# Kernel optimization log

Measured on AMD Instinct MI355X. Metric: run time of the kernel, lower is better.

## Reference

```python
import jax, jax.numpy as jnp
import numpy as np

B, N, D = 8, 1024, 768      # batch, n_patches, prototype dim
V, C, Hh = 30000, 512, 768  # vocab size, clip_text_dim, proj hidden dim
TEMPERATURE = 0.2
BN_EPS = 1e-5


def _l2norm(x, axis=-1, eps=1e-12):
    # matches torch F.normalize (clamp_min on the norm)
    n = jnp.linalg.norm(x, axis=axis, keepdims=True)
    return x / jnp.maximum(n, eps)


def setup_inputs() -> dict:
    key = jax.random.key(0)
    k = jax.random.split(key, 6)
    patch_tokens = jax.random.normal(k[0], (B, N, D), dtype=jnp.float32)
    vocab_clip_embeddings = jax.random.normal(k[1], (V, C), dtype=jnp.float32)
    # ProjectionHead params: Linear(C->Hh, no bias) + BN(Hh) + ReLU + Linear(Hh->D, bias)
    W1 = jax.random.normal(k[2], (C, Hh), dtype=jnp.float32) / np.sqrt(C)
    bn_gamma = jnp.ones((Hh,), dtype=jnp.float32)
    bn_beta = jnp.zeros((Hh,), dtype=jnp.float32)
    W2 = jax.random.normal(k[3], (Hh, D), dtype=jnp.float32) / np.sqrt(Hh)
    b2 = jnp.zeros((D,), dtype=jnp.float32)
    return {
        "patch_tokens": patch_tokens,
        "vocab_clip_embeddings": vocab_clip_embeddings,
        "W1": W1,
        "bn_gamma": bn_gamma,
        "bn_beta": bn_beta,
        "W2": W2,
        "b2": b2,
    }


def reference(patch_tokens, vocab_clip_embeddings, W1, bn_gamma, bn_beta, W2, b2):
    # vocab CLIP embeddings are L2-normalized at module init
    vocab = _l2norm(vocab_clip_embeddings)            # [V, C]
    # ProjectionHead (training-mode BatchNorm over the V "batch" dim)
    h = vocab @ W1                                    # [V, Hh]
    mean = jnp.mean(h, axis=0)
    var = jnp.var(h, axis=0)                          # biased, as torch BN uses
    h = (h - mean) * (bn_gamma / jnp.sqrt(var + BN_EPS)) + bn_beta
    h = jax.nn.relu(h)
    prototypes = _l2norm(h @ W2 + b2)                 # [V, D]
    # normalize patch tokens, compute patch-prototype logits
    pt = _l2norm(patch_tokens)                        # [B, N, D]
    patch_prototype_logits = jnp.einsum("bnd,vd->bnv", pt, prototypes)  # [B, N, V]
    vocab_logits = jnp.max(patch_prototype_logits, axis=1)              # [B, V]
    mixture_weights = jax.nn.softmax(vocab_logits / TEMPERATURE, axis=-1)
    return mixture_weights
```

## Files before the change

kernel.cpp:

```cpp
#include <hip/hip_runtime.h>
#include <hip/hip_bf16.h>
#include <cstdint>


#define CDIV(a,b) (((a)+(b)-1)/(b))

using bf16x8 = __attribute__((ext_vector_type(8))) __bf16;
using f32x4  = __attribute__((ext_vector_type(4))) float;
using u16x8  = __attribute__((ext_vector_type(8))) unsigned short;
using u32x4  = __attribute__((ext_vector_type(4))) unsigned;

__device__ __forceinline__ unsigned short f2bf(float x) {
  unsigned u = __float_as_uint(x);
  u += 0x7fffu + ((u >> 16) & 1u);
  return (unsigned short)(u >> 16);
}
__device__ __forceinline__ float bf2f(unsigned short b) {
  return __uint_as_float(((unsigned)b) << 16);
}
__device__ __forceinline__ unsigned fkey(float x) {
  unsigned u = __float_as_uint(x);
  return (u & 0x80000000u) ? ~u : (u | 0x80000000u);
}
__device__ __forceinline__ float fdec(unsigned k) {
  unsigned u = (k & 0x80000000u) ? (k ^ 0x80000000u) : ~k;
  return __uint_as_float(u);
}

template<int NT, int NXT, int EPI, int CPX>
__global__ __launch_bounds__(512, 1)
void gemm8p_kernel(const unsigned short* __restrict__ A,
                   const unsigned short* __restrict__ B,
                   unsigned short* __restrict__ Cout,
                   const float* __restrict__ bias,
                   float* __restrict__ faux,
                   unsigned* __restrict__ maxk,
                   int aclamp)
{
  constexpr int K = NT * 64;
  __shared__ __align__(16) unsigned short lds[8 * 8192];

  const int tid = threadIdx.x;
  const int w = tid >> 6, lane = tid & 63;
  const int lr = lane & 15, kg = lane >> 4;
  const int wr = w >> 2, wc = w & 3;

  const int bid = blockIdx.x;
  const int wg = CPX ? ((bid & 7) * CPX + (bid >> 3)) : bid;
  const long m0 = (long)(wg / NXT) * 256;
  const long n0 = (long)(wg % NXT) * 256;

  auto stage = [&](int slot, int tk, int mat, int h) {
    const unsigned short* src = mat ? B : A;
    const long row0 = mat ? n0 : m0;
    unsigned short* dst = lds + (((slot * 2) + mat) * 2 + h) * 8192;
#pragma unroll
    for (int ld = 0; ld < 2; ++ld) {
      const int lc  = ld * 512 + tid;
      long row = row0 + (lc >> 2);
      if (!mat && row > aclamp) row = aclamp;
      const int qc  = (lc & 3) ^ (((lc >> 2) >> 1) & 3);
      const unsigned short* gp = src + row * K + tk * 64 + h * 32 + qc * 8;
      __builtin_amdgcn_global_load_lds(
          (const __attribute__((address_space(1))) void*)gp,
          (__attribute__((address_space(3))) void*)(dst + (ld * 512 + (w << 6)) * 8),
          16, 0, 0);
    }
  };
  auto rdA = [&](int s, int h, int fm) -> bf16x8 {
    const int row = wr * 128 + fm * 16 + lr;
    const int pc  = kg ^ ((row >> 1) & 3);
    return *(const bf16x8*)(lds + ((s * 2 + 0) * 2 + h) * 8192 + row * 32 + pc * 8);
  };
  auto rdB = [&](int s, int h, int fn) -> bf16x8 {
    const int row = wc * 64 + fn * 16 + lr;
    const int pc  = kg ^ ((row >> 1) & 3);
    return *(const bf16x8*)(lds + ((s * 2 + 1) * 2 + h) * 8192 + row * 32 + pc * 8);
  };

  f32x4 acc[8][4];
#pragma unroll
  for (int i = 0; i < 8; ++i)
#pragma unroll
    for (int j = 0; j < 4; ++j) acc[i][j] = f32x4{0.f, 0.f, 0.f, 0.f};

  stage(0, 0, 0, 0); stage(0, 0, 1, 0); stage(0, 0, 0, 1);
  stage(0, 0, 1, 1); stage(1, 1, 0, 0); stage(1, 1, 1, 0);
  asm volatile("s_waitcnt vmcnt(8)" ::: "memory");
  __builtin_amdgcn_s_barrier();

  bf16x8 a[4], b[4];
  auto tile_body = [&](int t, int s) {
    const int t1c = (t + 1 < NT) ? t + 1 : NT - 1;
    const int t2c = (t + 2 < NT) ? t + 2 : NT - 1;
    const int s1  = s ^ 1;

#pragma unroll
    for (int i = 0; i < 4; ++i) a[i] = rdA(s, 0, i);
#pragma unroll
    for (int i = 0; i < 4; ++i) b[i] = rdB(s, 0, i);
    stage(s1, t1c, 0, 1);
    __builtin_amdgcn_s_barrier();
    asm volatile("s_waitcnt lgkmcnt(0)" ::: "memory");
    __builtin_amdgcn_sched_barrier(0);
    __builtin_amdgcn_s_setprio(1);
#pragma unroll
    for (int fm = 0; fm < 4; ++fm)
#pragma unroll
      for (int fn = 0; fn < 4; ++fn)
        acc[fm][fn] = __builtin_amdgcn_mfma_f32_16x16x32_bf16(a[fm], b[fn], acc[fm][fn], 0, 0, 0);
    __builtin_amdgcn_s_setprio(0);
    __builtin_amdgcn_sched_barrier(0);
    __builtin_amdgcn_s_barrier();

#pragma unroll
    for (int i = 0; i < 4; ++i) a[i] = rdA(s, 0, 4 + i);
    stage(s1, t1c, 1, 1);
    __builtin_amdgcn_s_barrier();
    asm volatile("s_waitcnt lgkmcnt(0)" ::: "memory");
    __builtin_amdgcn_sched_barrier(0);
    __builtin_amdgcn_s_setprio(1);
#pragma unroll
    for (int fm = 0; fm < 4; ++fm)
#pragma unroll
      for (int fn = 0; fn < 4; ++fn)
        acc[4 + fm][fn] = __builtin_amdgcn_mfma_f32_16x16x32_bf16(a[fm], b[fn], acc[4 + fm][fn], 0, 0, 0);
    __builtin_amdgcn_s_setprio(0);
    asm volatile("s_waitcnt vmcnt(8)" ::: "memory");
    __builtin_amdgcn_sched_barrier(0);
    __builtin_amdgcn_s_barrier();

#pragma unroll
    for (int i = 0; i < 4; ++i) a[i] = rdA(s, 1, i);
#pragma unroll
    for (int i = 0; i < 4; ++i) b[i] = rdB(s, 1, i);
    stage(s, t2c, 0, 0);
    __builtin_amdgcn_s_barrier();
    asm volatile("s_waitcnt lgkmcnt(0)" ::: "memory");
    __builtin_amdgcn_sched_barrier(0);
    __builtin_amdgcn_s_setprio(1);
#pragma unroll
    for (int fm = 0; fm < 4; ++fm)
#pragma unroll
      for (int fn = 0; fn < 4; ++fn)
        acc[fm][fn] = __builtin_amdgcn_mfma_f32_16x16x32_bf16(a[fm], b[fn], acc[fm][fn], 0, 0, 0);
    __builtin_amdgcn_s_setprio(0);
    __builtin_amdgcn_sched_barrier(0);
    __builtin_amdgcn_s_barrier();

#pragma unroll
    for (int i = 0; i < 4; ++i) a[i] = rdA(s, 1, 4 + i);
    stage(s, t2c, 1, 0);
    __builtin_amdgcn_s_barrier();
    asm volatile("s_waitcnt lgkmcnt(0)" ::: "memory");
    __builtin_amdgcn_sched_barrier(0);
    __builtin_amdgcn_s_setprio(1);
#pragma unroll
    for (int fm = 0; fm < 4; ++fm)
#pragma unroll
      for (int fn = 0; fn < 4; ++fn)
        acc[4 + fm][fn] = __builtin_amdgcn_mfma_f32_16x16x32_bf16(a[fm], b[fn], acc[4 + fm][fn], 0, 0, 0);
    __builtin_amdgcn_s_setprio(0);
    asm volatile("s_waitcnt vmcnt(8)" ::: "memory");
    __builtin_amdgcn_sched_barrier(0);
    __builtin_amdgcn_s_barrier();
  };

  for (int tt = 0; tt < NT; tt += 2) { tile_body(tt, 0); tile_body(tt + 1, 1); }

  if (EPI == 2) {
    const int bb = (int)(m0 >> 10);
#pragma unroll
    for (int fn = 0; fn < 4; ++fn) {
      float mx = acc[0][fn][0];
#pragma unroll
      for (int fm = 0; fm < 8; ++fm)
#pragma unroll
        for (int j = 0; j < 4; ++j) mx = fmaxf(mx, acc[fm][fn][j]);
      mx = fmaxf(mx, __shfl_xor(mx, 16));
      mx = fmaxf(mx, __shfl_xor(mx, 32));
      const long gn = n0 + wc * 64 + fn * 16 + lr;
      if (lane < 16)
        atomicMax(maxk + (long)bb * 30208 + gn, fkey(mx * faux[gn]));
    }
  } else if (EPI == 0) {
#pragma unroll
    for (int fm = 0; fm < 8; ++fm) {
      const long gmb = m0 + wr * 128 + fm * 16 + kg * 4;
#pragma unroll
      for (int fn = 0; fn < 4; ++fn) {
        const long gn = n0 + wc * 64 + fn * 16 + lr;
#pragma unroll
        for (int j = 0; j < 4; ++j)
          Cout[(gmb + j) * (NXT * 256) + gn] = f2bf(acc[fm][fn][j]);
      }
    }
#pragma unroll
    for (int fn = 0; fn < 4; ++fn) {
      const long gn = n0 + wc * 64 + fn * 16 + lr;
      float s = 0.f, q = 0.f;
#pragma unroll
      for (int fm = 0; fm < 8; ++fm) {
        const long gmb = m0 + wr * 128 + fm * 16 + kg * 4;
#pragma unroll
        for (int j = 0; j < 4; ++j) {
          if (gmb + j <= aclamp) {
            const float x = acc[fm][fn][j];
            s += x; q += x * x;
          }
        }
      }
      s += __shfl_xor(s, 16); s += __shfl_xor(s, 32);
      q += __shfl_xor(q, 16); q += __shfl_xor(q, 32);
      if (lane < 16) {
        atomicAdd(faux + gn, s);
        atomicAdd(faux + 768 + gn, q);
      }
    }
  } else {
    float bv[4];
#pragma unroll
    for (int fn = 0; fn < 4; ++fn) bv[fn] = bias[n0 + wc * 64 + fn * 16 + lr];
#pragma unroll
    for (int fm = 0; fm < 8; ++fm) {
      const long gmb = m0 + wr * 128 + fm * 16 + kg * 4;
#pragma unroll
      for (int j = 0; j < 4; ++j) {
        const long gm = gmb + j;
        float rs = 0.f;
#pragma unroll
        for (int fn = 0; fn < 4; ++fn) {
          const long gn = n0 + wc * 64 + fn * 16 + lr;
          const float x = acc[fm][fn][j] + bv[fn];
          Cout[gm * (NXT * 256) + gn] = f2bf(x);
          rs += x * x;
        }
        rs += __shfl_xor(rs, 1); rs += __shfl_xor(rs, 2);
        rs += __shfl_xor(rs, 4); rs += __shfl_xor(rs, 8);
        if (lr == 0) atomicAdd(faux + gm, rs);
      }
    }
  }
}

template<int BLOCK>
__global__ __launch_bounds__(BLOCK)
void rownorm_kernel(const float* __restrict__ in, unsigned short* __restrict__ out,
                    int cols)
{
  __shared__ float red[BLOCK / 64];
  const int row = blockIdx.x, tid = threadIdx.x;
  const int nch = cols / 4;

  float x[4];
  float ss = 0.f;
  if (tid < nch) {
    const f32x4 v = ((const f32x4*)(in + (size_t)row * cols))[tid];
#pragma unroll
    for (int j = 0; j < 4; ++j) { x[j] = v[j]; ss += x[j] * x[j]; }
  }
#pragma unroll
  for (int m = 32; m; m >>= 1) ss += __shfl_xor(ss, m);
  if ((tid & 63) == 0) red[tid >> 6] = ss;
  __syncthreads();
  float tot = 0.f;
#pragma unroll
  for (int i = 0; i < BLOCK / 64; ++i) tot += red[i];
  const float inv = 1.0f / fmaxf(sqrtf(tot), 1e-12f);

  if (tid < nch) {
    __attribute__((ext_vector_type(4))) unsigned short o;
#pragma unroll
    for (int j = 0; j < 4; ++j) o[j] = f2bf(x[j] * inv);
    ((decltype(o)*)(out + (size_t)row * cols))[tid] = o;
  }
}

__global__ __launch_bounds__(256)
void transpose2_kernel(const float* __restrict__ W1, const float* __restrict__ W2,
                       unsigned short* __restrict__ W1T, unsigned short* __restrict__ W2T)
{
  const int i = blockIdx.x * 256 + threadIdx.x;
  if (i < 512 * 768) {
    const int r = i / 768, c = i - r * 768;
    W1T[c * 512 + r] = f2bf(W1[i]);
  } else {
    const int k = i - 512 * 768;
    if (k < 768 * 768) {
      const int r = k / 768, c = k - r * 768;
      W2T[c * 768 + r] = f2bf(W2[k]);
    }
  }
}

__global__ __launch_bounds__(256)
void bnfinal_kernel(const float* __restrict__ sums, const float* __restrict__ gamma,
                    const float* __restrict__ beta, float* __restrict__ sc,
                    float* __restrict__ sh)
{
  const int ch = blockIdx.x * 256 + threadIdx.x;
  if (ch < 768) {
    const float invV = 1.0f / 30000.0f;
    const float mean = sums[ch] * invV;
    const float var  = sums[768 + ch] * invV - mean * mean;
    const float s    = gamma[ch] / sqrtf(var + 1e-5f);
    sc[ch] = s;
    sh[ch] = beta[ch] - mean * s;
  }
}

__global__ __launch_bounds__(256)
void bnapply_kernel(unsigned short* __restrict__ h, const float* __restrict__ sc,
                    const float* __restrict__ sh)
{
  const int total = 30000 * 96;
  for (int c = blockIdx.x * 256 + threadIdx.x; c < total; c += 2048 * 256) {
    const int ch = (c % 96) * 8;
    const u16x8 v = ((const u16x8*)h)[c];
    u16x8 o;
#pragma unroll
    for (int j = 0; j < 8; ++j) {
      const float y = fmaf(bf2f(v[j]), sc[ch + j], sh[ch + j]);
      o[j] = f2bf(fmaxf(y, 0.0f));
    }
    ((u16x8*)h)[c] = o;
  }
}

__global__ __launch_bounds__(256)
void rfin_kernel(const float* __restrict__ rsum, float* __restrict__ rnorm)
{
  const int v = blockIdx.x * 256 + threadIdx.x;
  if (v < 30208) rnorm[v] = 1.0f / fmaxf(sqrtf(rsum[v]), 1e-12f);
}

__global__ __launch_bounds__(256)
void smpart_kernel(const unsigned* __restrict__ mk, float* __restrict__ partsum)
{
  __shared__ float red[4];
  const int b = blockIdx.y;
  const unsigned* row = mk + (size_t)b * 30208 + blockIdx.x * 1000;
  float s = 0.f;
  for (int t = threadIdx.x; t < 1000; t += 256)
    s += expf((fdec(row[t]) - 1.0f) * 5.0f);
#pragma unroll
  for (int m = 32; m; m >>= 1) s += __shfl_xor(s, m);
  if ((threadIdx.x & 63) == 0) red[threadIdx.x >> 6] = s;
  __syncthreads();
  if (threadIdx.x == 0)
    atomicAdd(partsum + b, red[0] + red[1] + red[2] + red[3]);
}

__global__ __launch_bounds__(256)
void smfinal_kernel(const unsigned* __restrict__ mk, const float* __restrict__ partsum,
                    float* __restrict__ out)
{
  const int b = blockIdx.y;
  const int c = blockIdx.x * 256 + threadIdx.x;
  if (c < 3750) {
    const unsigned* row = mk + (size_t)b * 30208 + c * 8;
    const float inv = 1.0f / partsum[b];
    const u32x4 k0 = *(const u32x4*)row;
    const u32x4 k1 = *(const u32x4*)(row + 4);
    f32x4 o0, o1;
#pragma unroll
    for (int j = 0; j < 4; ++j) {
      o0[j] = expf((fdec(k0[j]) - 1.0f) * 5.0f) * inv;
      o1[j] = expf((fdec(k1[j]) - 1.0f) * 5.0f) * inv;
    }
    float* op = out + (size_t)b * 30000 + c * 8;
    *(f32x4*)op = o0;
    *(f32x4*)(op + 4) = o1;
  }
}

extern "C" void kernel_launch(void* const* d_in, const int* in_sizes, int n_in,
                              void* d_out, int out_size, void* d_ws, size_t ws_size,
                              hipStream_t stream)
{
  (void)in_sizes; (void)n_in; (void)out_size; (void)ws_size;
  const float* patch = (const float*)d_in[0];
  const float* vocab = (const float*)d_in[1];
  const float* W1    = (const float*)d_in[2];
  const float* gamma = (const float*)d_in[3];
  const float* beta  = (const float*)d_in[4];
  const float* W2    = (const float*)d_in[5];
  const float* b2    = (const float*)d_in[6];
  float* out = (float*)d_out;

  char* ws = (char*)d_ws;
  size_t off = 0;
  auto alloc = [&](size_t bytes) {
    char* p = ws + off;
    off += (bytes + 1023) & ~(size_t)1023;
    return p;
  };
  unsigned short* vocab_n = (unsigned short*)alloc(30000ull * 512 * 2);
  unsigned short* pt_n    = (unsigned short*)alloc(8192ull * 768 * 2);
  unsigned short* W1T     = (unsigned short*)alloc(768ull * 512 * 2);
  unsigned short* W2T     = (unsigned short*)alloc(768ull * 768 * 2);
  unsigned short* hbuf    = (unsigned short*)alloc(30208ull * 768 * 2);
  unsigned short* pbuf    = (unsigned short*)alloc(30208ull * 768 * 2);
  float* zbase = (float*)alloc((1536ull + 30208 + 8 + 8ull * 30208) * 4);
  float*    bnsums  = zbase;
  float*    rsum    = zbase + 1536;
  float*    partsum = zbase + 1536 + 30208;
  unsigned* maxkey  = (unsigned*)(zbase + 1536 + 30208 + 8);
  float*    bnsc    = (float*)alloc(768ull * 4);
  float*    bnsh    = (float*)alloc(768ull * 4);
  float*    rnorm   = (float*)alloc(30208ull * 4);

  hipMemsetAsync(zbase, 0, (1536ull + 30208 + 8 + 8ull * 30208) * 4, stream);

  transpose2_kernel<<<CDIV(512 * 768 + 768 * 768, 256), 256, 0, stream>>>(W1, W2, W1T, W2T);
  rownorm_kernel<256><<<30000, 256, 0, stream>>>(vocab, vocab_n, 512);
  rownorm_kernel<256><<<8192, 256, 0, stream>>>(patch, pt_n, 768);

  gemm8p_kernel<8, 3, 0, 0><<<354, 512, 0, stream>>>(
      vocab_n, W1T, hbuf, nullptr, bnsums, nullptr, 29999);
  bnfinal_kernel<<<3, 256, 0, stream>>>(bnsums, gamma, beta, bnsc, bnsh);
  bnapply_kernel<<<2048, 256, 0, stream>>>(hbuf, bnsc, bnsh);

  gemm8p_kernel<12, 3, 1, 0><<<354, 512, 0, stream>>>(
      hbuf, W2T, pbuf, b2, rsum, nullptr, 30207);
  rfin_kernel<<<118, 256, 0, stream>>>(rsum, rnorm);

  gemm8p_kernel<12, 118, 2, 472><<<3776, 512, 0, stream>>>(
      pt_n, pbuf, nullptr, nullptr, rnorm, maxkey, 8191);

  smpart_kernel<<<dim3(30, 8), 256, 0, stream>>>(maxkey, partsum);
  smfinal_kernel<<<dim3(15, 8), 256, 0, stream>>>(maxkey, partsum, out);
}
```

Baseline: 592.1 us.

## Use 128-row tiles for projection GEMMs to fill more CUs

Adds a separate gemm128 kernel with 128x256 output tiles for the two projection-head GEMMs, which doubles their grid from 354 to 708 workgroups. The aim is to fix under-occupancy, since 354 blocks at one block per CU leave the 256 CUs unevenly loaded. The new kernel also uses a finer per-K-half pipeline with smaller LDS. The big logits GEMM becomes its own specialised kernel with the clamp removed. Smaller tiles lower per-block reuse of B and raise total B traffic.

```diff
diff --git a/kernel.cpp b/kernel.cpp
--- a/kernel.cpp
+++ b/kernel.cpp
@@ -27,17 +27,13 @@
   return __uint_as_float(u);
 }
 
-template<int NT, int NXT, int EPI, int CPX>
 __global__ __launch_bounds__(512, 1)
-void gemm8p_kernel(const unsigned short* __restrict__ A,
-                   const unsigned short* __restrict__ B,
-                   unsigned short* __restrict__ Cout,
-                   const float* __restrict__ bias,
-                   float* __restrict__ faux,
-                   unsigned* __restrict__ maxk,
-                   int aclamp)
-{
-  constexpr int K = NT * 64;
+void gbig_kernel(const unsigned short* __restrict__ A,
+                 const unsigned short* __restrict__ B,
+                 const float* __restrict__ rnorm,
+                 unsigned* __restrict__ maxk)
+{
+  constexpr int K = 768, NT = 12, NXT = 118;
   __shared__ __align__(16) unsigned short lds[8 * 8192];
 
   const int tid = threadIdx.x;
@@ -46,7 +42,7 @@
   const int wr = w >> 2, wc = w & 3;
 
   const int bid = blockIdx.x;
-  const int wg = CPX ? ((bid & 7) * CPX + (bid >> 3)) : bid;
+  const int wg = (bid & 7) * 472 + (bid >> 3);
   const long m0 = (long)(wg / NXT) * 256;
   const long n0 = (long)(wg % NXT) * 256;
 
@@ -57,8 +53,7 @@
 #pragma unroll
     for (int ld = 0; ld < 2; ++ld) {
       const int lc  = ld * 512 + tid;
-      long row = row0 + (lc >> 2);
-      if (!mat && row > aclamp) row = aclamp;
+      const long row = row0 + (lc >> 2);
       const int qc  = (lc & 3) ^ (((lc >> 2) >> 1) & 3);
       const unsigned short* gp = src + row * K + tk * 64 + h * 32 + qc * 8;
       __builtin_amdgcn_global_load_lds(
@@ -168,31 +163,131 @@
 
   for (int tt = 0; tt < NT; tt += 2) { tile_body(tt, 0); tile_body(tt + 1, 1); }
 
-  if (EPI == 2) {
-    const int bb = (int)(m0 >> 10);
-#pragma unroll
-    for (int fn = 0; fn < 4; ++fn) {
-      float mx = acc[0][fn][0];
-#pragma unroll
-      for (int fm = 0; fm < 8; ++fm)
-#pragma unroll
-        for (int j = 0; j < 4; ++j) mx = fmaxf(mx, acc[fm][fn][j]);
-      mx = fmaxf(mx, __shfl_xor(mx, 16));
-      mx = fmaxf(mx, __shfl_xor(mx, 32));
-      const long gn = n0 + wc * 64 + fn * 16 + lr;
-      if (lane < 16)
-        atomicMax(maxk + (long)bb * 30208 + gn, fkey(mx * faux[gn]));
-    }
-  } else if (EPI == 0) {
-#pragma unroll
-    for (int fm = 0; fm < 8; ++fm) {
-      const long gmb = m0 + wr * 128 + fm * 16 + kg * 4;
+  const int bb = (int)(m0 >> 10);
+#pragma unroll
+  for (int fn = 0; fn < 4; ++fn) {
+    float mx = acc[0][fn][0];
+#pragma unroll
+    for (int fm = 0; fm < 8; ++fm)
+#pragma unroll
+      for (int j = 0; j < 4; ++j) mx = fmaxf(mx, acc[fm][fn][j]);
+    mx = fmaxf(mx, __shfl_xor(mx, 16));
+    mx = fmaxf(mx, __shfl_xor(mx, 32));
+    const long gn = n0 + wc * 64 + fn * 16 + lr;
+    if (lane < 16)
+      atomicMax(maxk + (long)bb * 30208 + gn, fkey(mx * rnorm[gn]));
+  }
+}
+
+template<int NT, int EPI>
+__global__ __launch_bounds__(512, 1)
+void gemm128_kernel(const unsigned short* __restrict__ A,
+                    const unsigned short* __restrict__ B,
+                    unsigned short* __restrict__ Cout,
+                    const float* __restrict__ bias,
+                    float* __restrict__ faux,
+                    int aclamp)
+{
+  constexpr int K = NT * 64;
+  __shared__ __align__(16) unsigned short lds[49152];
+
+  const int tid = threadIdx.x;
+  const int w = tid >> 6, lane = tid & 63;
+  const int lr = lane & 15, kg = lane >> 4;
+  const int wr = w >> 2, wc = w & 3;
+
+  const int wg = blockIdx.x;
+  const long m0 = (long)(wg / 3) * 128;
+  const long n0 = (long)(wg % 3) * 256;
+
+  auto stageA = [&](int slot, int tk, int h) {
+    unsigned short* dst = lds + (slot * 2 + h) * 4096;
+    long row = m0 + (tid >> 2);
+    if (row > aclamp) row = aclamp;
+    const int qc = (tid & 3) ^ ((tid >> 3) & 3);
+    const unsigned short* gp = A + row * K + tk * 64 + h * 32 + qc * 8;
+    __builtin_amdgcn_global_load_lds(
+        (const __attribute__((address_space(1))) void*)gp,
+        (__attribute__((address_space(3))) void*)(dst + (w << 6) * 8), 16, 0, 0);
+  };
+  auto stageB = [&](int slot, int tk, int h) {
+    unsigned short* dst = lds + 16384 + (slot * 2 + h) * 8192;
+#pragma unroll
+    for (int ld = 0; ld < 2; ++ld) {
+      const int lc = ld * 512 + tid;
+      const long row = n0 + (lc >> 2);
+      const int qc = (lc & 3) ^ (((lc >> 2) >> 1) & 3);
+      const unsigned short* gp = B + row * K + tk * 64 + h * 32 + qc * 8;
+      __builtin_amdgcn_global_load_lds(
+          (const __attribute__((address_space(1))) void*)gp,
+          (__attribute__((address_space(3))) void*)(dst + (ld * 512 + (w << 6)) * 8),
+          16, 0, 0);
+    }
+  };
+  auto rdA = [&](int s, int h, int fm) -> bf16x8 {
+    const int row = wr * 64 + fm * 16 + lr;
+    const int pc  = kg ^ ((row >> 1) & 3);
+    return *(const bf16x8*)(lds + (s * 2 + h) * 4096 + row * 32 + pc * 8);
+  };
+  auto rdB = [&](int s, int h, int fn) -> bf16x8 {
+    const int row = wc * 64 + fn * 16 + lr;
+    const int pc  = kg ^ ((row >> 1) & 3);
+    return *(const bf16x8*)(lds + 16384 + (s * 2 + h) * 8192 + row * 32 + pc * 8);
+  };
+
+  f32x4 acc[4][4];
+#pragma unroll
+  for (int i = 0; i < 4; ++i)
+#pragma unroll
+    for (int j = 0; j < 4; ++j) acc[i][j] = f32x4{0.f, 0.f, 0.f, 0.f};
+
+  stageA(0, 0, 0); stageB(0, 0, 0);
+  stageA(0, 0, 1); stageB(0, 0, 1);
+  stageA(1, 1, 0); stageB(1, 1, 0);
+  asm volatile("s_waitcnt vmcnt(6)" ::: "memory");
+  __builtin_amdgcn_s_barrier();
+
+  bf16x8 a[4], b[4];
+  auto phase = [&](int s, int h, int st_slot, int st_tk, int st_h) {
+#pragma unroll
+    for (int i = 0; i < 4; ++i) a[i] = rdA(s, h, i);
+#pragma unroll
+    for (int i = 0; i < 4; ++i) b[i] = rdB(s, h, i);
+    stageA(st_slot, st_tk, st_h);
+    stageB(st_slot, st_tk, st_h);
+    __builtin_amdgcn_s_barrier();
+    asm volatile("s_waitcnt lgkmcnt(0)" ::: "memory");
+    __builtin_amdgcn_sched_barrier(0);
+    __builtin_amdgcn_s_setprio(1);
+#pragma unroll
+    for (int fm = 0; fm < 4; ++fm)
+#pragma unroll
+      for (int fn = 0; fn < 4; ++fn)
+        acc[fm][fn] = __builtin_amdgcn_mfma_f32_16x16x32_bf16(a[fm], b[fn], acc[fm][fn], 0, 0, 0);
+    __builtin_amdgcn_s_setprio(0);
+    asm volatile("s_waitcnt vmcnt(6)" ::: "memory");
+    __builtin_amdgcn_sched_barrier(0);
+    __builtin_amdgcn_s_barrier();
+  };
+
+  for (int t = 0; t < NT; ++t) {
+    const int s = t & 1;
+    const int t1c = (t + 1 < NT) ? t + 1 : NT - 1;
+    const int t2c = (t + 2 < NT) ? t + 2 : NT - 1;
+    phase(s, 0, s ^ 1, t1c, 1);
+    phase(s, 1, s, t2c, 0);
+  }
+
+  if (EPI == 0) {
+#pragma unroll
+    for (int fm = 0; fm < 4; ++fm) {
+      const long gmb = m0 + wr * 64 + fm * 16 + kg * 4;
 #pragma unroll
       for (int fn = 0; fn < 4; ++fn) {
         const long gn = n0 + wc * 64 + fn * 16 + lr;
 #pragma unroll
         for (int j = 0; j < 4; ++j)
-          Cout[(gmb + j) * (NXT * 256) + gn] = f2bf(acc[fm][fn][j]);
+          Cout[(gmb + j) * 768 + gn] = f2bf(acc[fm][fn][j]);
       }
     }
 #pragma unroll
@@ -200,8 +295,8 @@
       const long gn = n0 + wc * 64 + fn * 16 + lr;
       float s = 0.f, q = 0.f;
 #pragma unroll
-      for (int fm = 0; fm < 8; ++fm) {
-        const long gmb = m0 + wr * 128 + fm * 16 + kg * 4;
+      for (int fm = 0; fm < 4; ++fm) {
+        const long gmb = m0 + wr * 64 + fm * 16 + kg * 4;
 #pragma unroll
         for (int j = 0; j < 4; ++j) {
           if (gmb + j <= aclamp) {
@@ -222,8 +317,8 @@
 #pragma unroll
     for (int fn = 0; fn < 4; ++fn) bv[fn] = bias[n0 + wc * 64 + fn * 16 + lr];
 #pragma unroll
-    for (int fm = 0; fm < 8; ++fm) {
-      const long gmb = m0 + wr * 128 + fm * 16 + kg * 4;
+    for (int fm = 0; fm < 4; ++fm) {
+      const long gmb = m0 + wr * 64 + fm * 16 + kg * 4;
 #pragma unroll
       for (int j = 0; j < 4; ++j) {
         const long gm = gmb + j;
@@ -232,7 +327,7 @@
         for (int fn = 0; fn < 4; ++fn) {
           const long gn = n0 + wc * 64 + fn * 16 + lr;
           const float x = acc[fm][fn][j] + bv[fn];
-          Cout[gm * (NXT * 256) + gn] = f2bf(x);
+          Cout[gm * 768 + gn] = f2bf(x);
           rs += x * x;
         }
         rs += __shfl_xor(rs, 1); rs += __shfl_xor(rs, 2);
@@ -416,17 +511,16 @@
   rownorm_kernel<256><<<30000, 256, 0, stream>>>(vocab, vocab_n, 512);
   rownorm_kernel<256><<<8192, 256, 0, stream>>>(patch, pt_n, 768);
 
-  gemm8p_kernel<8, 3, 0, 0><<<354, 512, 0, stream>>>(
-      vocab_n, W1T, hbuf, nullptr, bnsums, nullptr, 29999);
+  gemm128_kernel<8, 0><<<708, 512, 0, stream>>>(
+      vocab_n, W1T, hbuf, nullptr, bnsums, 29999);
   bnfinal_kernel<<<3, 256, 0, stream>>>(bnsums, gamma, beta, bnsc, bnsh);
   bnapply_kernel<<<2048, 256, 0, stream>>>(hbuf, bnsc, bnsh);
 
-  gemm8p_kernel<12, 3, 1, 0><<<354, 512, 0, stream>>>(
-      hbuf, W2T, pbuf, b2, rsum, nullptr, 30207);
+  gemm128_kernel<12, 1><<<708, 512, 0, stream>>>(
+      hbuf, W2T, pbuf, b2, rsum, 30207);
   rfin_kernel<<<118, 256, 0, stream>>>(rsum, rnorm);
 
-  gemm8p_kernel<12, 118, 2, 472><<<3776, 512, 0, stream>>>(
-      pt_n, pbuf, nullptr, nullptr, rnorm, maxkey, 8191);
+  gbig_kernel<<<3776, 512, 0, stream>>>(pt_n, pbuf, rnorm, maxkey);
 
   smpart_kernel<<<dim3(30, 8), 256, 0, stream>>>(maxkey, partsum);
   smfinal_kernel<<<dim3(15, 8), 256, 0, stream>>>(maxkey, partsum, out);
```

Result: slower. 623.7 us (+5.4%).
